# Performance work log

Hardware: AMD Instinct MI355X
Metric: run time of the kernel (lower is better)

## Reference

```python
import jax, jax.numpy as jnp
import numpy as np

WINDOW = (2, 8, 8)
SHIFT = (1, 4, 4)
HEADS = 6
DIM = 96
B, T, H, W = 2, 8, 128, 128
SCALE = (DIM // HEADS) ** -0.5


def _layernorm(x, g, b, eps=1e-5):
    m = jnp.mean(x, axis=-1, keepdims=True)
    v = jnp.var(x, axis=-1, keepdims=True)
    return (x - m) * jax.lax.rsqrt(v + eps) * g + b


def _window_partition(x):
    b, t, h, w, c = x.shape
    wd, wh, ww = WINDOW
    x = x.reshape(b, t // wd, wd, h // wh, wh, w // ww, ww, c)
    x = x.transpose(0, 1, 3, 5, 2, 4, 6, 7)
    return x.reshape(-1, wd * wh * ww, c)


def _window_reverse(win, b, t, h, w):
    wd, wh, ww = WINDOW
    c = win.shape[-1]
    x = win.reshape(b, t // wd, h // wh, w // ww, wd, wh, ww, c)
    x = x.transpose(0, 1, 4, 2, 5, 3, 6, 7)
    return x.reshape(b, t, h, w, c)


def _build_mask():
    wd, wh, ww = WINDOW
    sd, sh, sw = SHIFT
    img = np.zeros((1, T, H, W, 1), dtype=np.float32)
    cnt = 0
    for ds in (slice(0, -wd), slice(-wd, -sd), slice(-sd, None)):
        for hs in (slice(0, -wh), slice(-wh, -sh), slice(-sh, None)):
            for ws_ in (slice(0, -ww), slice(-ww, -sw), slice(-sw, None)):
                img[:, ds, hs, ws_, :] = cnt
                cnt += 1
    mw = _window_partition(jnp.asarray(img)).squeeze(-1)  # (nW, N)
    diff = mw[:, None, :] - mw[:, :, None]
    return jnp.where(diff != 0, -100.0, 0.0).astype(jnp.float32)


def setup_inputs() -> dict:
    key = jax.random.key(0)
    ks = jax.random.split(key, 8)
    c = DIM
    hid = 4 * c
    s = 0.02
    return {
        "x": jax.random.normal(ks[0], (B, T, H, W, c), dtype=jnp.float32),
        "attn_mask": _build_mask(),
        "g1": jnp.ones((c,), jnp.float32),
        "b1": jnp.zeros((c,), jnp.float32),
        "w_qkv": jax.random.normal(ks[1], (3 * c, c), jnp.float32) * s,
        "b_qkv": jnp.zeros((3 * c,), jnp.float32),
        "w_proj": jax.random.normal(ks[2], (c, c), jnp.float32) * s,
        "b_proj": jnp.zeros((c,), jnp.float32),
        "g2": jnp.ones((c,), jnp.float32),
        "b2": jnp.zeros((c,), jnp.float32),
        "w_fc1": jax.random.normal(ks[3], (hid, c), jnp.float32) * s,
        "b_fc1": jnp.zeros((hid,), jnp.float32),
        "w_fc2": jax.random.normal(ks[4], (c, hid), jnp.float32) * s,
        "b_fc2": jnp.zeros((c,), jnp.float32),
    }


def reference(x, attn_mask, g1, b1, w_qkv, b_qkv, w_proj, b_proj, g2, b2, w_fc1, b_fc1, w_fc2, b_fc2):
    b, t, h, w, c = x.shape
    shortcut = x
    y = _layernorm(x, g1, b1)
    # cyclic shift (dims divide window sizes evenly, so no padding needed)
    y = jnp.roll(y, shift=(-SHIFT[0], -SHIFT[1], -SHIFT[2]), axis=(1, 2, 3))
    xw = _window_partition(y)  # (b*nW, N, c)
    Bn, N, _ = xw.shape
    hd = c // HEADS
    qkv = xw @ w_qkv.T + b_qkv  # (Bn, N, 3c)
    qkv = qkv.reshape(Bn, N, 3, HEADS, hd).transpose(2, 0, 3, 1, 4)
    q, k, v = qkv[0], qkv[1], qkv[2]  # (Bn, heads, N, hd)
    attn = jnp.einsum("bhnd,bhmd->bhnm", q * SCALE, k)
    nW = attn_mask.shape[0]
    attn = attn.reshape(Bn // nW, nW, HEADS, N, N) + attn_mask[None, :, None]
    attn = jax.nn.softmax(attn.reshape(Bn, HEADS, N, N), axis=-1)
    out = jnp.einsum("bhnm,bhmd->bhnd", attn, v)
    out = out.transpose(0, 2, 1, 3).reshape(Bn, N, c)
    out = out @ w_proj.T + b_proj
    y = _window_reverse(out, b, t, h, w)
    y = jnp.roll(y, shift=SHIFT, axis=(1, 2, 3))
    y = shortcut + y
    # MLP: Linear -> GELU (exact, matches nn.GELU) -> Linear
    z = _layernorm(y, g2, b2)
    z = jax.nn.gelu(z @ w_fc1.T + b_fc1, approximate=False)
    z = z @ w_fc2.T + b_fc2
    return y + z
```

## Files before the change

kernel.cpp:

```cpp
#include <hip/hip_runtime.h>
#include <math.h>

typedef __bf16 bf16x8 __attribute__((ext_vector_type(8)));
typedef unsigned short u16x8 __attribute__((ext_vector_type(8)));
typedef unsigned short u16x4 __attribute__((ext_vector_type(4)));
typedef float f32x4 __attribute__((ext_vector_type(4)));

__device__ __forceinline__ float bf2f(unsigned short u) {
  union { unsigned u; float f; } v; v.u = ((unsigned)u) << 16; return v.f;
}
__device__ __forceinline__ unsigned short f2bf(float f) {
  union { float f; unsigned u; } v; v.f = f;
  unsigned r = v.u + 0x7fffu + ((v.u >> 16) & 1u);
  return (unsigned short)(r >> 16);
}
__device__ __forceinline__ unsigned pk_bf16(float lo, float hi) {
  unsigned r;
  asm("v_cvt_pk_bf16_f32 %0, %1, %2" : "=v"(r) : "v"(lo), "v"(hi));
  return r;
}
__device__ __forceinline__ void cfence() { asm volatile("" ::: "memory"); }

__device__ __forceinline__ bf16x8 ld8(const unsigned short* p) {
  return __builtin_bit_cast(bf16x8, *(const u16x8*)p);
}
__device__ __forceinline__ bf16x8 ld8f(const float* p) {
  f32x4 a = *(const f32x4*)p;
  f32x4 b = *(const f32x4*)(p + 4);
  u16x8 u;
#pragma unroll
  for (int i = 0; i < 4; ++i) { u[i] = f2bf(a[i]); u[4 + i] = f2bf(b[i]); }
  return __builtin_bit_cast(bf16x8, u);
}
__device__ __forceinline__ float ldS(const void* p, int isf, size_t i) {
  return isf ? ((const float*)p)[i] : bf2f(((const unsigned short*)p)[i]);
}
__device__ __forceinline__ bf16x8 ld8G(const void* p, int isf, size_t i) {
  return isf ? ld8f((const float*)p + i) : ld8((const unsigned short*)p + i);
}
__device__ __forceinline__ void stO(void* p, int isf, size_t i, float v) {
  if (isf) ((float*)p)[i] = v; else ((unsigned short*)p)[i] = f2bf(v);
}
__device__ __forceinline__ bf16x8 zero8() {
  u16x8 z;
#pragma unroll
  for (int i = 0; i < 8; ++i) z[i] = 0;
  return __builtin_bit_cast(bf16x8, z);
}
__device__ __forceinline__ f32x4 fzero4() {
  f32x4 z; z[0] = z[1] = z[2] = z[3] = 0.f; return z;
}
__device__ __forceinline__ f32x4 mfma16(bf16x8 a, bf16x8 b, f32x4 c) {
  return __builtin_amdgcn_mfma_f32_16x16x32_bf16(a, b, c, 0, 0, 0);
}
__device__ __forceinline__ float scrub(float v) {
  return fminf(fmaxf(v, -1e6f), 1e6f);
}
__device__ __forceinline__ void st_pk8(unsigned short* p, const float* v) {
  uint4 w;
  w.x = pk_bf16(v[0], v[1]); w.y = pk_bf16(v[2], v[3]);
  w.z = pk_bf16(v[4], v[5]); w.w = pk_bf16(v[6], v[7]);
  *(u16x8*)p = __builtin_bit_cast(u16x8, w);
}
__device__ __forceinline__ void st_pk4(unsigned short* p, float a, float b, float c, float d) {
  uint2 w; w.x = pk_bf16(a, b); w.y = pk_bf16(c, d);
  *(u16x4*)p = __builtin_bit_cast(u16x4, w);
}
__device__ __forceinline__ float gelu_f(float x) {
  float ax = fabsf(x);
  float t = __builtin_amdgcn_rcpf(1.0f + 0.3275911f * ax);
  float poly = t * (0.254829592f + t * (-0.284496736f + t * (1.421413741f +
               t * (-1.453152027f + t * 1.061405429f))));
  float er = 1.0f - poly * __expf(-ax * ax);
  er = copysignf(er, x);
  return 0.5f * x * (1.0f + er);
}

#define C_DIM 96
#define XO_STR 104
#define QH_STR 24
#define VP_STR 136
#define SCRW 2176
#define QHW 3072
#define A_HALF 13312
#define QB_HALF 18432

__global__ void dtype_sniff(const unsigned short* __restrict__ x, int* __restrict__ flag) {
  int lane = threadIdx.x;
  int weird = 0;
#pragma unroll
  for (int k = 0; k < 4; ++k) {
    unsigned short w = x[lane * 4 + k];
    int e = (w >> 7) & 0xFF;
    if (e >= 0xC0 || (e != 0 && e <= 0x30)) weird++;
  }
#pragma unroll
  for (int d = 1; d < 64; d <<= 1) weird += __shfl_xor(weird, d, 64);
  if (lane == 0) *flag = (weird > 16) ? 1 : 0;
}

__global__ __launch_bounds__(768, 3) void swin_attn_kernel(
    const void* __restrict__ x,
    const void* __restrict__ g1,
    const void* __restrict__ b1,
    const void* __restrict__ w_qkv,
    const void* __restrict__ b_qkv,
    const void* __restrict__ w_proj,
    const void* __restrict__ b_proj,
    void* __restrict__ y,
    const int* __restrict__ flag)
{
  __shared__ __align__(16) unsigned short sm_A[2 * A_HALF];
  __shared__ __align__(16) unsigned short sm_qB[2 * QB_HALF];
  __shared__ int sm_tok[2 * 128];
  __shared__ int sm_cls[2 * 128];
  __shared__ int sm_nu[2][2];

  const int isf = *flag;
  const int tid = threadIdx.x;
  const int half = (tid >= 384) ? 1 : 0;
  const int t = tid - half * 384;
  unsigned short* smA = sm_A + half * A_HALF;
  unsigned short* smQ = sm_qB + half * QB_HALF;
  int* tokp = sm_tok + half * 128;
  int* clsp = sm_cls + half * 128;
  float* sm_red = (float*)smQ;

  const int win = blockIdx.x * 2 + half;
  const int b = win >> 10;
  const int rem = win & 1023;
  const int ti = rem >> 8, hi = (rem >> 4) & 15, wi = rem & 15;

  {
    const int n = t & 127;
    const int part = t >> 7;
    const int td = n >> 6, hh = (n >> 3) & 7, ww = n & 7;
    const int tt = ti * 2 + td, h = hi * 8 + hh, w = wi * 8 + ww;
    const int ts = (tt + 1) & 7, hs = (h + 4) & 127, ws = (w + 4) & 127;
    const int tok = ((b * 8 + ts) * 128 + hs) * 128 + ws;
    if (part == 0) {
      tokp[n] = tok;
      int ct = (tt < 6) ? 0 : (tt - 5);
      int ch = (h < 120) ? 0 : ((h < 124) ? 1 : 2);
      int cw = (w < 120) ? 0 : ((w < 124) ? 1 : 2);
      int cls = ct * 9 + ch * 3 + cw;
      clsp[n] = cls;
      int t0 = ti * 2;
      int ct0 = (t0 < 6) ? 0 : (t0 - 5);
      int ch0 = (hi < 15) ? 0 : 1;
      int cw0 = (wi < 15) ? 0 : 1;
      int cls0 = ct0 * 9 + ch0 * 3 + cw0;
      unsigned long long bal = __ballot(cls != cls0);
      if ((t & 63) == 0) sm_nu[half][t >> 6] = (bal != 0ULL) ? 1 : 0;
    }
    float v[32];
    if (isf) {
      const float* xp = (const float*)x + (size_t)tok * C_DIM + part * 32;
      f32x4 raw[8];
#pragma unroll
      for (int i = 0; i < 8; ++i) raw[i] = ((const f32x4*)xp)[i];
#pragma unroll
      for (int i = 0; i < 32; ++i) v[i] = raw[i >> 2][i & 3];
    } else {
      const unsigned short* xp = (const unsigned short*)x + (size_t)tok * C_DIM + part * 32;
      u16x8 raw[4];
#pragma unroll
      for (int i = 0; i < 4; ++i) raw[i] = ((const u16x8*)xp)[i];
#pragma unroll
      for (int i = 0; i < 32; ++i) v[i] = bf2f(raw[i >> 3][i & 7]);
    }
    float s = 0.f, s2 = 0.f;
#pragma unroll
    for (int i = 0; i < 32; ++i) {
      v[i] = scrub(v[i]);
      s += v[i]; s2 += v[i] * v[i];
    }
    sm_red[part * 128 + n] = s;
    sm_red[(3 + part) * 128 + n] = s2;
    __syncthreads();
    float tsum = sm_red[0 * 128 + n] + sm_red[1 * 128 + n] + sm_red[2 * 128 + n];
    float tsq  = sm_red[3 * 128 + n] + sm_red[4 * 128 + n] + sm_red[5 * 128 + n];
    float mean = tsum * (1.0f / 96.0f);
    float var = fmaxf(tsq * (1.0f / 96.0f) - mean * mean, 0.0f);
    float rstd = rsqrtf(var + 1e-5f);
    float o[32];
#pragma unroll
    for (int i = 0; i < 32; ++i) {
      int c = part * 32 + i;
      o[i] = (v[i] - mean) * rstd * ldS(g1, isf, c) + ldS(b1, isf, c);
    }
#pragma unroll
    for (int k = 0; k < 4; ++k)
      st_pk8(smA + n * XO_STR + part * 32 + k * 8, &o[k * 8]);
  }
  __syncthreads();

  const int wv = t >> 6;
  const int lane = t & 63;
  const int quad = lane >> 4;
  const int l16 = lane & 15;
  unsigned short* scr = smA + wv * SCRW;
  unsigned short* qh  = smQ + wv * QHW;

  bf16x8 az[3][8];
#pragma unroll
  for (int kt = 0; kt < 3; ++kt)
#pragma unroll
    for (int mt = 0; mt < 8; ++mt)
      az[kt][mt] = ld8(smA + (mt * 16 + l16) * XO_STR + kt * 32 + quad * 8);

  bf16x8 bwQ[3], bwK[3], bwV[3];
  {
    const int jq = wv * 16 + l16;
#pragma unroll
    for (int kt = 0; kt < 3; ++kt) {
      bwQ[kt] = ld8G(w_qkv, isf, (size_t)jq * C_DIM + kt * 32 + quad * 8);
      bwK[kt] = ld8G(w_qkv, isf, (size_t)(C_DIM + jq) * C_DIM + kt * 32 + quad * 8);
      bwV[kt] = ld8G(w_qkv, isf, (size_t)(2 * C_DIM + jq) * C_DIM + kt * 32 + quad * 8);
    }
  }

  {
    float bias[4];
#pragma unroll
    for (int r = 0; r < 4; ++r) bias[r] = ldS(b_qkv, isf, wv * 16 + quad * 4 + r);
    for (int mt = 0; mt < 8; ++mt) {
      f32x4 acc = fzero4();
#pragma unroll
      for (int kt = 0; kt < 3; ++kt) acc = mfma16(bwQ[kt], az[kt][mt], acc);
      st_pk4(&qh[(mt * 16 + l16) * QH_STR + quad * 4],
             (acc[0] + bias[0]) * 0.25f, (acc[1] + bias[1]) * 0.25f,
             (acc[2] + bias[2]) * 0.25f, (acc[3] + bias[3]) * 0.25f);
    }
  }
  __syncthreads();

  bf16x8 bk[8], bv[4];
  {
    float bias[4];
#pragma unroll
    for (int r = 0; r < 4; ++r) bias[r] = ldS(b_qkv, isf, C_DIM + wv * 16 + quad * 4 + r);
    for (int mt = 0; mt < 8; ++mt) {
      f32x4 acc = fzero4();
#pragma unroll
      for (int kt = 0; kt < 3; ++kt) acc = mfma16(bwK[kt], az[kt][mt], acc);
      st_pk4(&scr[(mt * 16 + l16) * 16 + quad * 4],
             acc[0] + bias[0], acc[1] + bias[1], acc[2] + bias[2], acc[3] + bias[3]);
    }
    cfence();
#pragma unroll
    for (int nt = 0; nt < 8; ++nt)
      bk[nt] = (quad < 2) ? ld8(scr + (nt * 16 + l16) * 16 + quad * 8) : zero8();
    cfence();
  }
  {
    const float bias = ldS(b_qkv, isf, 2 * C_DIM + wv * 16 + l16);
    for (int mt = 0; mt < 8; ++mt) {
      f32x4 acc = fzero4();
#pragma unroll
      for (int kt = 0; kt < 3; ++kt) acc = mfma16(az[kt][mt], bwV[kt], acc);
#pragma unroll
      for (int r = 0; r < 4; ++r)
        scr[l16 * VP_STR + (mt * 16 + quad * 4 + r)] = f2bf(acc[r] + bias);
    }
    cfence();
#pragma unroll
    for (int kt = 0; kt < 4; ++kt)
      bv[kt] = ld8(scr + l16 * VP_STR + kt * 32 + quad * 8);
    cfence();
  }

  bf16x8 bp[3];
  {
    const int jcol = wv * 16 + l16;
#pragma unroll
    for (int kt = 0; kt < 3; ++kt)
      bp[kt] = ld8G(w_proj, isf, (size_t)jcol * C_DIM + kt * 32 + quad * 8);
  }

  {
    const int nu = sm_nu[half][0] | sm_nu[half][1];
    for (int qt = 0; qt < 8; ++qt) {
      bf16x8 bq = (quad < 2) ? ld8(qh + (qt * 16 + l16) * QH_STR + quad * 8) : zero8();
      f32x4 s[8];
      __builtin_amdgcn_s_setprio(1);
#pragma unroll
      for (int nt = 0; nt < 8; ++nt) s[nt] = mfma16(bk[nt], bq, fzero4());
      __builtin_amdgcn_s_setprio(0);
      if (nu) {
        const int rc = clsp[qt * 16 + l16];
#pragma unroll
        for (int nt = 0; nt < 8; ++nt) {
          int4 cc = *(const int4*)&clsp[nt * 16 + quad * 4];
          s[nt][0] += (cc.x != rc) ? -100.0f : 0.0f;
          s[nt][1] += (cc.y != rc) ? -100.0f : 0.0f;
          s[nt][2] += (cc.z != rc) ? -100.0f : 0.0f;
          s[nt][3] += (cc.w != rc) ? -100.0f : 0.0f;
        }
      }
      float m = s[0][0];
#pragma unroll
      for (int nt = 0; nt < 8; ++nt)
#pragma unroll
        for (int r = 0; r < 4; ++r) m = fmaxf(m, s[nt][r]);
      m = fmaxf(m, __shfl_xor(m, 16, 64));
      m = fmaxf(m, __shfl_xor(m, 32, 64));
      float sum = 0.f;
#pragma unroll
      for (int nt = 0; nt < 8; ++nt)
#pragma unroll
        for (int r = 0; r < 4; ++r) {
          float e = __expf(s[nt][r] - m);
          s[nt][r] = e; sum += e;
        }
      sum += __shfl_xor(sum, 16, 64);
      sum += __shfl_xor(sum, 32, 64);
      const float inv = 1.0f / sum;
      cfence();
#pragma unroll
      for (int nt = 0; nt < 8; ++nt)
        st_pk4(&scr[l16 * VP_STR + nt * 16 + quad * 4],
               s[nt][0] * inv, s[nt][1] * inv, s[nt][2] * inv, s[nt][3] * inv);
      cfence();
      f32x4 o = fzero4();
      __builtin_amdgcn_s_setprio(1);
#pragma unroll
      for (int kt = 0; kt < 4; ++kt)
        o = mfma16(bv[kt], ld8(scr + l16 * VP_STR + kt * 32 + quad * 8), o);
      __builtin_amdgcn_s_setprio(0);
      st_pk4(&qh[(qt * 16 + l16) * QH_STR + quad * 4], o[0], o[1], o[2], o[3]);
    }
  }
  __syncthreads();

  {
    const int jcol = wv * 16 + l16;
    const float bias = ldS(b_proj, isf, jcol);
    for (int mt = 0; mt < 8; ++mt) {
      f32x4 acc = fzero4();
#pragma unroll
      for (int kt = 0; kt < 3; ++kt) {
        const int c0 = kt * 32 + quad * 8;
        const int h2 = c0 >> 4, off = c0 & 15;
        bf16x8 a = ld8(smQ + h2 * QHW + (mt * 16 + l16) * QH_STR + off);
        acc = mfma16(a, bp[kt], acc);
      }
#pragma unroll
      for (int r = 0; r < 4; ++r) {
        int row = mt * 16 + quad * 4 + r;
        size_t addr = (size_t)tokp[row] * C_DIM + jcol;
        stO(y, isf, addr, scrub(ldS(x, isf, addr)) + acc[r] + bias);
      }
    }
  }
}

__global__ __launch_bounds__(768, 3) void swin_mlp_kernel(
    const void* __restrict__ g2,
    const void* __restrict__ b2,
    const void* __restrict__ w_fc1,
    const void* __restrict__ b_fc1,
    const void* __restrict__ w_fc2,
    const void* __restrict__ b_fc2,
    void* __restrict__ yout,
    const int* __restrict__ flag)
{
  __shared__ __align__(16) unsigned short sm_z[2 * A_HALF];
  __shared__ __align__(16) unsigned short sm_h[2 * A_HALF];

  const int isf = *flag;
  const int tid = threadIdx.x;
  const int half = (tid >= 384) ? 1 : 0;
  const int t = tid - half * 384;
  unsigned short* smz = sm_z + half * A_HALF;
  unsigned short* smh = sm_h + half * A_HALF;
  float* sm_red = (float*)smh;
  const size_t tok0 = ((size_t)blockIdx.x * 2 + half) * 128;

  {
    const int n = t & 127;
    const int part = t >> 7;
    float v[32];
    if (isf) {
      const float* yp = (const float*)yout + (tok0 + n) * C_DIM + part * 32;
      f32x4 raw[8];
#pragma unroll
      for (int i = 0; i < 8; ++i) raw[i] = ((const f32x4*)yp)[i];
#pragma unroll
      for (int i = 0; i < 32; ++i) v[i] = raw[i >> 2][i & 3];
    } else {
      const unsigned short* yp = (const unsigned short*)yout + (tok0 + n) * C_DIM + part * 32;
      u16x8 raw[4];
#pragma unroll
      for (int i = 0; i < 4; ++i) raw[i] = ((const u16x8*)yp)[i];
#pragma unroll
      for (int i = 0; i < 32; ++i) v[i] = bf2f(raw[i >> 3][i & 7]);
    }
    float s = 0.f, s2 = 0.f;
#pragma unroll
    for (int i = 0; i < 32; ++i) { s += v[i]; s2 += v[i] * v[i]; }
    sm_red[part * 128 + n] = s;
    sm_red[(3 + part) * 128 + n] = s2;
    __syncthreads();
    float tsum = sm_red[0 * 128 + n] + sm_red[1 * 128 + n] + sm_red[2 * 128 + n];
    float tsq  = sm_red[3 * 128 + n] + sm_red[4 * 128 + n] + sm_red[5 * 128 + n];
    float mean = tsum * (1.0f / 96.0f);
    float var = fmaxf(tsq * (1.0f / 96.0f) - mean * mean, 0.0f);
    float rstd = rsqrtf(var + 1e-5f);
    float o[32];
#pragma unroll
    for (int i = 0; i < 32; ++i) {
      int c = part * 32 + i;
      o[i] = (v[i] - mean) * rstd * ldS(g2, isf, c) + ldS(b2, isf, c);
    }
#pragma unroll
    for (int k = 0; k < 4; ++k)
      st_pk8(smz + n * XO_STR + part * 32 + k * 8, &o[k * 8]);
  }
  __syncthreads();

  const int wv = t >> 6;
  const int lane = t & 63;
  const int quad = lane >> 4;
  const int l16 = lane & 15;
  const int jcol_o = wv * 16 + l16;

  bf16x8 az[3][8];
#pragma unroll
  for (int kt = 0; kt < 3; ++kt)
#pragma unroll
    for (int mt = 0; mt < 8; ++mt)
      az[kt][mt] = ld8(smz + (mt * 16 + l16) * XO_STR + kt * 32 + quad * 8);

  f32x4 acc2[8];
#pragma unroll
  for (int mt = 0; mt < 8; ++mt) acc2[mt] = fzero4();

  for (int c = 0; c < 4; ++c) {
    const int hb = c * 96 + wv * 16;
    bf16x8 bw1[3], bw2[3];
#pragma unroll
    for (int kt = 0; kt < 3; ++kt) {
      bw1[kt] = ld8G(w_fc1, isf, (size_t)(hb + l16) * C_DIM + kt * 32 + quad * 8);
      bw2[kt] = ld8G(w_fc2, isf, (size_t)jcol_o * 384 + c * 96 + kt * 32 + quad * 8);
    }
    float b1v[4];
#pragma unroll
    for (int r = 0; r < 4; ++r) b1v[r] = ldS(b_fc1, isf, hb + quad * 4 + r);
#pragma unroll
    for (int mt = 0; mt < 8; ++mt) {
      f32x4 acc = fzero4();
#pragma unroll
      for (int kt = 0; kt < 3; ++kt) acc = mfma16(bw1[kt], az[kt][mt], acc);
      float g[4];
#pragma unroll
      for (int r = 0; r < 4; ++r) g[r] = gelu_f(acc[r] + b1v[r]);
      st_pk4(&smh[(mt * 16 + l16) * XO_STR + wv * 16 + quad * 4],
             g[0], g[1], g[2], g[3]);
    }
    __syncthreads();
#pragma unroll
    for (int mt = 0; mt < 8; ++mt) {
#pragma unroll
      for (int kt = 0; kt < 3; ++kt) {
        bf16x8 a = ld8(smh + (mt * 16 + l16) * XO_STR + kt * 32 + quad * 8);
        acc2[mt] = mfma16(a, bw2[kt], acc2[mt]);
      }
    }
    if (c < 3) __syncthreads();
  }

  {
    const float bias = ldS(b_fc2, isf, jcol_o);
#pragma unroll
    for (int mt = 0; mt < 8; ++mt) {
#pragma unroll
      for (int r = 0; r < 4; ++r) {
        int row = mt * 16 + quad * 4 + r;
        size_t addr = (tok0 + row) * C_DIM + jcol_o;
        stO(yout, isf, addr, ldS(yout, isf, addr) + acc2[mt][r] + bias);
      }
    }
  }
}

extern "C" void kernel_launch(void* const* d_in, const int* in_sizes, int n_in,
                              void* d_out, int out_size, void* d_ws, size_t ws_size,
                              hipStream_t stream) {
  const void* x      = d_in[0];
  const void* g1     = d_in[2];
  const void* b1     = d_in[3];
  const void* w_qkv  = d_in[4];
  const void* b_qkv  = d_in[5];
  const void* w_proj = d_in[6];
  const void* b_proj = d_in[7];
  const void* g2     = d_in[8];
  const void* b2     = d_in[9];
  const void* w_fc1  = d_in[10];
  const void* b_fc1  = d_in[11];
  const void* w_fc2  = d_in[12];
  const void* b_fc2  = d_in[13];
  int* flag = (int*)d_ws;

  dtype_sniff<<<1, 64, 0, stream>>>((const unsigned short*)x, flag);
  swin_attn_kernel<<<1024, 768, 0, stream>>>(x, g1, b1, w_qkv, b_qkv, w_proj, b_proj, d_out, flag);
  swin_mlp_kernel<<<1024, 768, 0, stream>>>(g2, b2, w_fc1, b_fc1, w_fc2, b_fc2, d_out, flag);
}
```

Measured before the change: 592.4 us.

## Fuse attention and MLP into one Swin block kernel keeping residual in registers

Merges the attention and MLP kernels into a single kernel. The post-projection residual stays in registers (transposed MFMA output so each lane holds four contiguous channels), and LayerNorm2 is computed through a cross-wave shared-memory reduction. The MLP then runs on the same token tile, and the final output is written once with vectorized stores. This removes the intermediate y write and read and one kernel launch, at the cost of higher register pressure and extra barriers in one larger kernel.

```diff
diff --git a/kernel.cpp b/kernel.cpp
--- a/kernel.cpp
+++ b/kernel.cpp
@@ -37,9 +37,6 @@
 }
 __device__ __forceinline__ bf16x8 ld8G(const void* p, int isf, size_t i) {
   return isf ? ld8f((const float*)p + i) : ld8((const unsigned short*)p + i);
-}
-__device__ __forceinline__ void stO(void* p, int isf, size_t i, float v) {
-  if (isf) ((float*)p)[i] = v; else ((unsigned short*)p)[i] = f2bf(v);
 }
 __device__ __forceinline__ bf16x8 zero8() {
   u16x8 z;
@@ -99,7 +96,7 @@
   if (lane == 0) *flag = (weird > 16) ? 1 : 0;
 }
 
-__global__ __launch_bounds__(768, 3) void swin_attn_kernel(
+__global__ __launch_bounds__(768, 3) void swin_block_kernel(
     const void* __restrict__ x,
     const void* __restrict__ g1,
     const void* __restrict__ b1,
@@ -107,6 +104,12 @@
     const void* __restrict__ b_qkv,
     const void* __restrict__ w_proj,
     const void* __restrict__ b_proj,
+    const void* __restrict__ g2,
+    const void* __restrict__ b2,
+    const void* __restrict__ w_fc1,
+    const void* __restrict__ b_fc1,
+    const void* __restrict__ w_fc2,
+    const void* __restrict__ b_fc2,
     void* __restrict__ y,
     const int* __restrict__ flag)
 {
@@ -333,152 +336,142 @@
   }
   __syncthreads();
 
-  {
-    const int jcol = wv * 16 + l16;
-    const float bias = ldS(b_proj, isf, jcol);
-    for (int mt = 0; mt < 8; ++mt) {
+  f32x4 yv[8];
+  {
+    float biasp[4];
+#pragma unroll
+    for (int r = 0; r < 4; ++r) biasp[r] = ldS(b_proj, isf, wv * 16 + quad * 4 + r);
+    for (int nt = 0; nt < 8; ++nt) {
       f32x4 acc = fzero4();
 #pragma unroll
       for (int kt = 0; kt < 3; ++kt) {
         const int c0 = kt * 32 + quad * 8;
         const int h2 = c0 >> 4, off = c0 & 15;
-        bf16x8 a = ld8(smQ + h2 * QHW + (mt * 16 + l16) * QH_STR + off);
-        acc = mfma16(a, bp[kt], acc);
-      }
-#pragma unroll
-      for (int r = 0; r < 4; ++r) {
-        int row = mt * 16 + quad * 4 + r;
-        size_t addr = (size_t)tokp[row] * C_DIM + jcol;
-        stO(y, isf, addr, scrub(ldS(x, isf, addr)) + acc[r] + bias);
-      }
-    }
-  }
-}
-
-__global__ __launch_bounds__(768, 3) void swin_mlp_kernel(
-    const void* __restrict__ g2,
-    const void* __restrict__ b2,
-    const void* __restrict__ w_fc1,
-    const void* __restrict__ b_fc1,
-    const void* __restrict__ w_fc2,
-    const void* __restrict__ b_fc2,
-    void* __restrict__ yout,
-    const int* __restrict__ flag)
-{
-  __shared__ __align__(16) unsigned short sm_z[2 * A_HALF];
-  __shared__ __align__(16) unsigned short sm_h[2 * A_HALF];
-
-  const int isf = *flag;
-  const int tid = threadIdx.x;
-  const int half = (tid >= 384) ? 1 : 0;
-  const int t = tid - half * 384;
-  unsigned short* smz = sm_z + half * A_HALF;
-  unsigned short* smh = sm_h + half * A_HALF;
-  float* sm_red = (float*)smh;
-  const size_t tok0 = ((size_t)blockIdx.x * 2 + half) * 128;
-
-  {
-    const int n = t & 127;
-    const int part = t >> 7;
-    float v[32];
-    if (isf) {
-      const float* yp = (const float*)yout + (tok0 + n) * C_DIM + part * 32;
-      f32x4 raw[8];
-#pragma unroll
-      for (int i = 0; i < 8; ++i) raw[i] = ((const f32x4*)yp)[i];
-#pragma unroll
-      for (int i = 0; i < 32; ++i) v[i] = raw[i >> 2][i & 3];
-    } else {
-      const unsigned short* yp = (const unsigned short*)yout + (tok0 + n) * C_DIM + part * 32;
-      u16x8 raw[4];
-#pragma unroll
-      for (int i = 0; i < 4; ++i) raw[i] = ((const u16x8*)yp)[i];
-#pragma unroll
-      for (int i = 0; i < 32; ++i) v[i] = bf2f(raw[i >> 3][i & 7]);
-    }
+        bf16x8 bo = ld8(smQ + h2 * QHW + (nt * 16 + l16) * QH_STR + off);
+        acc = mfma16(bp[kt], bo, acc);
+      }
+      const size_t base = (size_t)tokp[nt * 16 + l16] * C_DIM + wv * 16 + quad * 4;
+      f32x4 xr;
+      if (isf) {
+        xr = *(const f32x4*)((const float*)x + base);
+      } else {
+        u16x4 u = *(const u16x4*)((const unsigned short*)x + base);
+#pragma unroll
+        for (int j = 0; j < 4; ++j) xr[j] = bf2f(u[j]);
+      }
+#pragma unroll
+      for (int r = 0; r < 4; ++r)
+        yv[nt][r] = scrub(xr[r]) + acc[r] + biasp[r];
+    }
+  }
+  __syncthreads();
+
+  float* fred = (float*)(smQ + 13312);
+  float* fmr  = (float*)(smQ + 16384);
+  {
+    for (int nt = 0; nt < 8; ++nt) {
+      float s  = yv[nt][0] + yv[nt][1] + yv[nt][2] + yv[nt][3];
+      float s2 = yv[nt][0] * yv[nt][0] + yv[nt][1] * yv[nt][1]
+               + yv[nt][2] * yv[nt][2] + yv[nt][3] * yv[nt][3];
+      s  += __shfl_xor(s, 16, 64);  s2 += __shfl_xor(s2, 16, 64);
+      s  += __shfl_xor(s, 32, 64);  s2 += __shfl_xor(s2, 32, 64);
+      if (quad == 0) {
+        float2 p; p.x = s; p.y = s2;
+        ((float2*)fred)[(nt * 16 + l16) * 6 + wv] = p;
+      }
+    }
+  }
+  __syncthreads();
+  if (t < 128) {
     float s = 0.f, s2 = 0.f;
 #pragma unroll
-    for (int i = 0; i < 32; ++i) { s += v[i]; s2 += v[i] * v[i]; }
-    sm_red[part * 128 + n] = s;
-    sm_red[(3 + part) * 128 + n] = s2;
-    __syncthreads();
-    float tsum = sm_red[0 * 128 + n] + sm_red[1 * 128 + n] + sm_red[2 * 128 + n];
-    float tsq  = sm_red[3 * 128 + n] + sm_red[4 * 128 + n] + sm_red[5 * 128 + n];
-    float mean = tsum * (1.0f / 96.0f);
-    float var = fmaxf(tsq * (1.0f / 96.0f) - mean * mean, 0.0f);
-    float rstd = rsqrtf(var + 1e-5f);
-    float o[32];
-#pragma unroll
-    for (int i = 0; i < 32; ++i) {
-      int c = part * 32 + i;
-      o[i] = (v[i] - mean) * rstd * ldS(g2, isf, c) + ldS(b2, isf, c);
-    }
-#pragma unroll
-    for (int k = 0; k < 4; ++k)
-      st_pk8(smz + n * XO_STR + part * 32 + k * 8, &o[k * 8]);
-  }
-  __syncthreads();
-
-  const int wv = t >> 6;
-  const int lane = t & 63;
-  const int quad = lane >> 4;
-  const int l16 = lane & 15;
-  const int jcol_o = wv * 16 + l16;
-
-  bf16x8 az[3][8];
-#pragma unroll
-  for (int kt = 0; kt < 3; ++kt)
-#pragma unroll
-    for (int mt = 0; mt < 8; ++mt)
-      az[kt][mt] = ld8(smz + (mt * 16 + l16) * XO_STR + kt * 32 + quad * 8);
+    for (int w = 0; w < 6; ++w) {
+      float2 p = ((float2*)fred)[t * 6 + w];
+      s += p.x; s2 += p.y;
+    }
+    float mean = s * (1.0f / 96.0f);
+    float var = fmaxf(s2 * (1.0f / 96.0f) - mean * mean, 0.0f);
+    float2 mr; mr.x = mean; mr.y = rsqrtf(var + 1e-5f);
+    ((float2*)fmr)[t] = mr;
+  }
+  __syncthreads();
+
+  {
+    float g2v[4], b2v[4];
+#pragma unroll
+    for (int r = 0; r < 4; ++r) {
+      g2v[r] = ldS(g2, isf, wv * 16 + quad * 4 + r);
+      b2v[r] = ldS(b2, isf, wv * 16 + quad * 4 + r);
+    }
+    for (int nt = 0; nt < 8; ++nt) {
+      float2 mr = ((float2*)fmr)[nt * 16 + l16];
+      float z0 = (yv[nt][0] - mr.x) * mr.y * g2v[0] + b2v[0];
+      float z1 = (yv[nt][1] - mr.x) * mr.y * g2v[1] + b2v[1];
+      float z2 = (yv[nt][2] - mr.x) * mr.y * g2v[2] + b2v[2];
+      float z3 = (yv[nt][3] - mr.x) * mr.y * g2v[3] + b2v[3];
+      st_pk4(&smA[(nt * 16 + l16) * XO_STR + wv * 16 + quad * 4], z0, z1, z2, z3);
+    }
+  }
+  __syncthreads();
 
   f32x4 acc2[8];
 #pragma unroll
-  for (int mt = 0; mt < 8; ++mt) acc2[mt] = fzero4();
+  for (int nt = 0; nt < 8; ++nt) acc2[nt] = fzero4();
+  unsigned short* hbuf = smQ;
 
   for (int c = 0; c < 4; ++c) {
     const int hb = c * 96 + wv * 16;
-    bf16x8 bw1[3], bw2[3];
+    bf16x8 a1[3], a2[3];
 #pragma unroll
     for (int kt = 0; kt < 3; ++kt) {
-      bw1[kt] = ld8G(w_fc1, isf, (size_t)(hb + l16) * C_DIM + kt * 32 + quad * 8);
-      bw2[kt] = ld8G(w_fc2, isf, (size_t)jcol_o * 384 + c * 96 + kt * 32 + quad * 8);
+      a1[kt] = ld8G(w_fc1, isf, (size_t)(hb + l16) * C_DIM + kt * 32 + quad * 8);
+      a2[kt] = ld8G(w_fc2, isf, (size_t)(wv * 16 + l16) * 384 + c * 96 + kt * 32 + quad * 8);
     }
     float b1v[4];
 #pragma unroll
     for (int r = 0; r < 4; ++r) b1v[r] = ldS(b_fc1, isf, hb + quad * 4 + r);
 #pragma unroll
-    for (int mt = 0; mt < 8; ++mt) {
+    for (int nt = 0; nt < 8; ++nt) {
       f32x4 acc = fzero4();
 #pragma unroll
-      for (int kt = 0; kt < 3; ++kt) acc = mfma16(bw1[kt], az[kt][mt], acc);
-      float g[4];
-#pragma unroll
-      for (int r = 0; r < 4; ++r) g[r] = gelu_f(acc[r] + b1v[r]);
-      st_pk4(&smh[(mt * 16 + l16) * XO_STR + wv * 16 + quad * 4],
-             g[0], g[1], g[2], g[3]);
+      for (int kt = 0; kt < 3; ++kt) {
+        bf16x8 bz = ld8(smA + (nt * 16 + l16) * XO_STR + kt * 32 + quad * 8);
+        acc = mfma16(a1[kt], bz, acc);
+      }
+      float g0 = gelu_f(acc[0] + b1v[0]);
+      float g1v = gelu_f(acc[1] + b1v[1]);
+      float g2x = gelu_f(acc[2] + b1v[2]);
+      float g3 = gelu_f(acc[3] + b1v[3]);
+      st_pk4(&hbuf[(nt * 16 + l16) * XO_STR + wv * 16 + quad * 4], g0, g1v, g2x, g3);
     }
     __syncthreads();
 #pragma unroll
-    for (int mt = 0; mt < 8; ++mt) {
+    for (int nt = 0; nt < 8; ++nt) {
 #pragma unroll
       for (int kt = 0; kt < 3; ++kt) {
-        bf16x8 a = ld8(smh + (mt * 16 + l16) * XO_STR + kt * 32 + quad * 8);
-        acc2[mt] = mfma16(a, bw2[kt], acc2[mt]);
+        bf16x8 bh = ld8(hbuf + (nt * 16 + l16) * XO_STR + kt * 32 + quad * 8);
+        acc2[nt] = mfma16(a2[kt], bh, acc2[nt]);
       }
     }
     if (c < 3) __syncthreads();
   }
 
   {
-    const float bias = ldS(b_fc2, isf, jcol_o);
-#pragma unroll
-    for (int mt = 0; mt < 8; ++mt) {
-#pragma unroll
-      for (int r = 0; r < 4; ++r) {
-        int row = mt * 16 + quad * 4 + r;
-        size_t addr = (tok0 + row) * C_DIM + jcol_o;
-        stO(yout, isf, addr, ldS(yout, isf, addr) + acc2[mt][r] + bias);
+    float b2o[4];
+#pragma unroll
+    for (int r = 0; r < 4; ++r) b2o[r] = ldS(b_fc2, isf, wv * 16 + quad * 4 + r);
+    for (int nt = 0; nt < 8; ++nt) {
+      const size_t base = (size_t)tokp[nt * 16 + l16] * C_DIM + wv * 16 + quad * 4;
+      if (isf) {
+        f32x4 o4;
+#pragma unroll
+        for (int r = 0; r < 4; ++r) o4[r] = yv[nt][r] + acc2[nt][r] + b2o[r];
+        *(f32x4*)((float*)y + base) = o4;
+      } else {
+        u16x4 u;
+#pragma unroll
+        for (int r = 0; r < 4; ++r) u[r] = f2bf(yv[nt][r] + acc2[nt][r] + b2o[r]);
+        *(u16x4*)((unsigned short*)y + base) = u;
       }
     }
   }
@@ -503,6 +496,7 @@
   int* flag = (int*)d_ws;
 
   dtype_sniff<<<1, 64, 0, stream>>>((const unsigned short*)x, flag);
-  swin_attn_kernel<<<1024, 768, 0, stream>>>(x, g1, b1, w_qkv, b_qkv, w_proj, b_proj, d_out, flag);
-  swin_mlp_kernel<<<1024, 768, 0, stream>>>(g2, b2, w_fc1, b_fc1, w_fc2, b_fc2, d_out, flag);
-}
+  swin_block_kernel<<<1024, 768, 0, stream>>>(
+      x, g1, b1, w_qkv, b_qkv, w_proj, b_proj,
+      g2, b2, w_fc1, b_fc1, w_fc2, b_fc2, d_out, flag);
+}
```

New measurement: 506.4 us. 1.17x faster.
